# Optimization experiments

Measured on AMD Instinct MI355X. Metric: run time of the kernel, lower is better.

## Reference

```python
import jax, jax.numpy as jnp
import numpy as np

TOP_K = 2
EPS = 1e-06


def setup_inputs() -> dict:
    key = jax.random.key(0)
    k1, k2 = jax.random.split(key)
    x = jax.random.normal(k1, (4, 8192, 1024), dtype=jnp.float32)
    # nn.Linear weight: [num_experts, d_model]
    W = jax.random.normal(k2, (64, 1024), dtype=jnp.float32) * (1.0 / np.sqrt(1024))
    return {"x": x, "W": W}


def reference(x, W):
    # router logits: (b, s, e)
    logits = jnp.einsum('bsd,ed->bse', x, W)
    # top-k selection (values sorted descending, like torch.topk)
    top_vals, top_idx = jax.lax.top_k(logits, TOP_K)
    top_gates = jax.nn.softmax(top_vals, axis=-1)
    # load-balance loss over full softmax probs
    probs = jax.nn.softmax(logits, axis=-1)
    avg_probs = probs.mean(axis=(0, 1))  # (e,)
    # torch.std defaults to unbiased (ddof=1)
    loss = (jnp.std(avg_probs, ddof=1) / (avg_probs.mean() + EPS)) ** 2
    return (top_idx, top_gates, loss)
```

## Files before the change

### kernel.cpp

```cpp
#include <hip/hip_runtime.h>
#include <math.h>
#include <stdint.h>


constexpr int DMODEL = 1024;
constexpr int NEXP   = 64;
constexpr int BM     = 64;
constexpr int BK     = 64;
constexpr int NTOK   = 32768;
constexpr int NTILE  = DMODEL / BK;

constexpr int XS   = 0;
constexpr int XSB  = 64 * 64 * 4;
constexpr int WS   = 32768;
constexpr int WSB  = 3 * 64 * 64 * 2;
constexpr int WCMP = 64 * 64 * 2;
constexpr int LSTR = 68 * 4;

typedef __attribute__((ext_vector_type(8))) short short8;
typedef __attribute__((ext_vector_type(4))) float f32x4;

__device__ __forceinline__ void gload16(const float* g, char* l) {
    __builtin_amdgcn_global_load_lds(
        (const __attribute__((address_space(1))) unsigned int*)g,
        (__attribute__((address_space(3))) unsigned int*)l,
        16, 0, 0);
}

__device__ __forceinline__ void split3(float x, short& h, short& m, short& l) {
    uint32_t u  = __float_as_uint(x);
    uint32_t uh = u & 0xffff0000u;
    float    r  = x - __uint_as_float(uh);
    uint32_t ur = __float_as_uint(r);
    uint32_t um = ur & 0xffff0000u;
    float    r2 = r - __uint_as_float(um);
    h = (short)(uh >> 16);
    m = (short)(um >> 16);
    l = (short)(__float_as_uint(r2) >> 16);
}

__global__ __launch_bounds__(512, 2) void router_kernel(
    const float* __restrict__ x, const float* __restrict__ W,
    float* __restrict__ out, float* __restrict__ expert_sums)
{
    __shared__ __align__(16) char smem[81920];

    const int tid  = threadIdx.x;
    const int lane = tid & 63;
    const int w    = tid >> 6;
    const int mt   = w & 3;
    const int kh   = w >> 2;
    const int tok0 = blockIdx.x * BM;

    f32x4 acc[4];
#pragma unroll
    for (int nt = 0; nt < 4; ++nt) acc[nt] = (f32x4){0.f, 0.f, 0.f, 0.f};

    auto stageX = [&](int buf, int tile) {
#pragma unroll
        for (int i = 0; i < 2; ++i) {
            const int r0 = w * 8 + i * 4;
            const int r  = r0 + (lane >> 4);
            const int c  = lane & 15;
            const float* src = x + (size_t)(tok0 + r) * DMODEL + tile * BK
                                 + ((c ^ (r & 15)) << 2);
            gload16(src, smem + XS + buf * XSB + r0 * 256 + (lane << 4));
        }
    };

    const int we  = tid >> 3;
    const int wc  = tid & 7;
    const int wph = wc ^ (we & 7);
    const float* wgp = W + (size_t)we * DMODEL + wc * 8;

    auto convW = [&](int buf, float4 a, float4 b) {
        short8 sH, sM, sL;
        float v[8] = {a.x, a.y, a.z, a.w, b.x, b.y, b.z, b.w};
#pragma unroll
        for (int j = 0; j < 8; ++j) {
            short h, m, l; split3(v[j], h, m, l);
            sH[j] = h; sM[j] = m; sL[j] = l;
        }
        char* d = smem + WS + buf * WSB + we * 128 + wph * 16;
        *reinterpret_cast<short8*>(d)             = sH;
        *reinterpret_cast<short8*>(d + WCMP)      = sM;
        *reinterpret_cast<short8*>(d + 2 * WCMP)  = sL;
    };

    stageX(0, 0);
    {
        float4 a = *reinterpret_cast<const float4*>(wgp);
        float4 b = *reinterpret_cast<const float4*>(wgp + 4);
        convW(0, a, b);
    }
    __syncthreads();

    int buf = 0;
    for (int tile = 0; tile < NTILE; ++tile) {
        float4 wa, wb;
        if (tile + 1 < NTILE) {
            stageX(buf ^ 1, tile + 1);
            wa = *reinterpret_cast<const float4*>(wgp + (tile + 1) * BK);
            wb = *reinterpret_cast<const float4*>(wgp + (tile + 1) * BK + 4);
        }

        {
            const int ks = kh;
            const int rl = mt * 16 + (lane & 15);
            const int c0 = ks * 8 + (lane >> 4) * 2;
            const char* xrow = smem + XS + buf * XSB + rl * 256;
            const float4 xa = *reinterpret_cast<const float4*>(
                xrow + ((c0 ^ (lane & 15)) << 4));
            const float4 xb = *reinterpret_cast<const float4*>(
                xrow + (((c0 + 1) ^ (lane & 15)) << 4));
            short8 aH, aM, aL;
            {
                float v[8] = {xa.x, xa.y, xa.z, xa.w, xb.x, xb.y, xb.z, xb.w};
#pragma unroll
                for (int j = 0; j < 8; ++j) {
                    short h, m, l; split3(v[j], h, m, l);
                    aH[j] = h; aM[j] = m; aL[j] = l;
                }
            }
#pragma unroll
            for (int nt = 0; nt < 4; ++nt) {
                const int ef = nt * 16 + (lane & 15);
                const int q  = ks * 4 + (lane >> 4);
                const char* wrow = smem + WS + buf * WSB + ef * 128
                                 + ((q ^ (ef & 7)) << 4);
                const short8 bH = *reinterpret_cast<const short8*>(wrow);
                const short8 bM = *reinterpret_cast<const short8*>(wrow + WCMP);
                const short8 bL = *reinterpret_cast<const short8*>(wrow + 2 * WCMP);
                acc[nt] = __builtin_amdgcn_mfma_f32_16x16x32_bf16(aH, bH, acc[nt], 0, 0, 0);
                acc[nt] = __builtin_amdgcn_mfma_f32_16x16x32_bf16(aH, bM, acc[nt], 0, 0, 0);
                acc[nt] = __builtin_amdgcn_mfma_f32_16x16x32_bf16(aM, bH, acc[nt], 0, 0, 0);
                acc[nt] = __builtin_amdgcn_mfma_f32_16x16x32_bf16(aH, bL, acc[nt], 0, 0, 0);
                acc[nt] = __builtin_amdgcn_mfma_f32_16x16x32_bf16(aM, bM, acc[nt], 0, 0, 0);
                acc[nt] = __builtin_amdgcn_mfma_f32_16x16x32_bf16(aL, bH, acc[nt], 0, 0, 0);
            }
        }

        if (tile + 1 < NTILE) convW(buf ^ 1, wa, wb);
        __syncthreads();
        buf ^= 1;
    }

    if (kh == 0) {
#pragma unroll
        for (int nt = 0; nt < 4; ++nt)
#pragma unroll
            for (int r = 0; r < 4; ++r) {
                const int t = mt * 16 + (lane >> 4) * 4 + r;
                const int e = nt * 16 + (lane & 15);
                *reinterpret_cast<float*>(smem + t * LSTR + e * 4) = acc[nt][r];
            }
    }
    __syncthreads();
    if (kh == 1) {
#pragma unroll
        for (int nt = 0; nt < 4; ++nt)
#pragma unroll
            for (int r = 0; r < 4; ++r) {
                const int t = mt * 16 + (lane >> 4) * 4 + r;
                const int e = nt * 16 + (lane & 15);
                float* p = reinterpret_cast<float*>(smem + t * LSTR + e * 4);
                *p += acc[nt][r];
            }
    }
    __syncthreads();

    float* maxArr = reinterpret_cast<float*>(smem + 18432);
    float* invArr = reinterpret_cast<float*>(smem + 18688);
    float* psum   = reinterpret_cast<float*>(smem + 18944);

    if (tid < BM) {
        const char* lrow = smem + tid * LSTR;
        float4 L[16];
#pragma unroll
        for (int i = 0; i < 16; ++i)
            L[i] = *reinterpret_cast<const float4*>(lrow + i * 16);

        float mx = -INFINITY;
#pragma unroll
        for (int i = 0; i < 16; ++i)
            mx = fmaxf(mx, fmaxf(fmaxf(L[i].x, L[i].y), fmaxf(L[i].z, L[i].w)));

        float v0 = -INFINITY, v1 = -INFINITY;
        int   i0 = NEXP, i1 = NEXP;
        float s = 0.f;
#pragma unroll
        for (int i = 0; i < 16; ++i) {
            const float vv[4] = {L[i].x, L[i].y, L[i].z, L[i].w};
#pragma unroll
            for (int c = 0; c < 4; ++c) {
                const float v = vv[c];
                const int  gi = i * 4 + c;
                s += __expf(v - mx);
                if (v > v0) { v1 = v0; i1 = i0; v0 = v; i0 = gi; }
                else if (v > v1) { v1 = v; i1 = gi; }
            }
        }
        maxArr[tid] = mx;
        invArr[tid] = 1.0f / s;

        const float q = __expf(v1 - v0);
        const float d = 1.0f + q;
        const size_t tok = (size_t)tok0 + tid;
        reinterpret_cast<float2*>(out)[tok]            = make_float2((float)i0, (float)i1);
        reinterpret_cast<float2*>(out + 2 * NTOK)[tok] = make_float2(1.0f / d, q / d);
    }
    __syncthreads();

    {
        const int e = tid & 63, grp = tid >> 6;
        float s = 0.f;
#pragma unroll
        for (int i = 0; i < 8; ++i) {
            const int t = grp * 8 + i;
            const float lg = *reinterpret_cast<const float*>(smem + t * LSTR + e * 4);
            s += __expf(lg - maxArr[t]) * invArr[t];
        }
        psum[grp * 64 + e] = s;
    }
    __syncthreads();
    if (tid < 64) {
        float s = 0.f;
#pragma unroll
        for (int g = 0; g < 8; ++g) s += psum[g * 64 + tid];
        atomicAdd(&expert_sums[tid], s);
    }
}

__global__ void loss_kernel(const float* __restrict__ sums, float* __restrict__ out)
{
    const int lane = threadIdx.x;
    float pv = sums[lane] * (1.0f / (float)NTOK);
    float m = pv;
#pragma unroll
    for (int off = 32; off; off >>= 1) m += __shfl_xor(m, off, 64);
    m *= (1.0f / (float)NEXP);
    float d = pv - m;
    float v = d * d;
#pragma unroll
    for (int off = 32; off; off >>= 1) v += __shfl_xor(v, off, 64);
    v *= (1.0f / (float)(NEXP - 1));
    if (lane == 0) {
        float stdv = sqrtf(v);
        float r = stdv / (m + 1e-6f);
        out[4 * NTOK] = r * r;
    }
}

extern "C" void kernel_launch(void* const* d_in, const int* in_sizes, int n_in,
                              void* d_out, int out_size, void* d_ws, size_t ws_size,
                              hipStream_t stream)
{
    const float* x = (const float*)d_in[0];
    const float* W = (const float*)d_in[1];
    float* out  = (float*)d_out;
    float* sums = (float*)d_ws;

    hipMemsetAsync(d_ws, 0, NEXP * sizeof(float), stream);

    hipLaunchKernelGGL(router_kernel, dim3(NTOK / BM), dim3(512), 0, stream,
                       x, W, out, sums);
    hipLaunchKernelGGL(loss_kernel, dim3(1), dim3(64), 0, stream, sums, out);
}
```

Measured before the change: 53.02 us.

## Pre-split W into bf16 triples once and stream tiles via direct-to-LDS loads

Adds a small pre-pass kernel that splits W into hi/mid/lo bf16 components, writes them to workspace in the swizzled LDS tile layout, and has the router kernel load W tiles with global_load_lds instead of converting W per block. This removes the redundant per-block W conversion and its register round-trip. The loop sync changes to explicit vmcnt waits plus raw s_barrier, so the next tile's loads stay in flight during the MFMA work. The cost is an extra kernel launch and workspace traffic. A fallback keeps the old path when the workspace is too small.

```diff
diff --git a/kernel.cpp b/kernel.cpp
--- a/kernel.cpp
+++ b/kernel.cpp
@@ -17,10 +17,13 @@
 constexpr int WCMP = 64 * 64 * 2;
 constexpr int LSTR = 68 * 4;
 
+constexpr size_t WSPLIT_OFF   = 256;
+constexpr size_t WSPLIT_BYTES = (size_t)NTILE * WSB;
+
 typedef __attribute__((ext_vector_type(8))) short short8;
 typedef __attribute__((ext_vector_type(4))) float f32x4;
 
-__device__ __forceinline__ void gload16(const float* g, char* l) {
+__device__ __forceinline__ void gload16(const void* g, void* l) {
     __builtin_amdgcn_global_load_lds(
         (const __attribute__((address_space(1))) unsigned int*)g,
         (__attribute__((address_space(3))) unsigned int*)l,
@@ -39,8 +42,31 @@
     l = (short)(__float_as_uint(r2) >> 16);
 }
 
+__global__ void wsplit_kernel(const float* __restrict__ W, char* __restrict__ dst)
+{
+    const int g = blockIdx.x * 256 + threadIdx.x;
+    const int e = g >> 7;
+    const int c = g & 127;
+    const int tile = c >> 3;
+    const int q    = c & 7;
+    const float* src = W + (size_t)e * DMODEL + c * 8;
+    const float4 a = *reinterpret_cast<const float4*>(src);
+    const float4 b = *reinterpret_cast<const float4*>(src + 4);
+    short8 sH, sM, sL;
+    const float v[8] = {a.x, a.y, a.z, a.w, b.x, b.y, b.z, b.w};
+#pragma unroll
+    for (int j = 0; j < 8; ++j) {
+        short h, m, l; split3(v[j], h, m, l);
+        sH[j] = h; sM[j] = m; sL[j] = l;
+    }
+    char* base = dst + (size_t)tile * WSB + e * 128 + ((q ^ (e & 7)) << 4);
+    *reinterpret_cast<short8*>(base)            = sH;
+    *reinterpret_cast<short8*>(base + WCMP)     = sM;
+    *reinterpret_cast<short8*>(base + 2 * WCMP) = sL;
+}
+
 __global__ __launch_bounds__(512, 2) void router_kernel(
-    const float* __restrict__ x, const float* __restrict__ W,
+    const float* __restrict__ x, const char* __restrict__ wsAll,
     float* __restrict__ out, float* __restrict__ expert_sums)
 {
     __shared__ __align__(16) char smem[81920];
@@ -67,42 +93,28 @@
             gload16(src, smem + XS + buf * XSB + r0 * 256 + (lane << 4));
         }
     };
-
-    const int we  = tid >> 3;
-    const int wc  = tid & 7;
-    const int wph = wc ^ (we & 7);
-    const float* wgp = W + (size_t)we * DMODEL + wc * 8;
-
-    auto convW = [&](int buf, float4 a, float4 b) {
-        short8 sH, sM, sL;
-        float v[8] = {a.x, a.y, a.z, a.w, b.x, b.y, b.z, b.w};
-#pragma unroll
-        for (int j = 0; j < 8; ++j) {
-            short h, m, l; split3(v[j], h, m, l);
-            sH[j] = h; sM[j] = m; sL[j] = l;
-        }
-        char* d = smem + WS + buf * WSB + we * 128 + wph * 16;
-        *reinterpret_cast<short8*>(d)             = sH;
-        *reinterpret_cast<short8*>(d + WCMP)      = sM;
-        *reinterpret_cast<short8*>(d + 2 * WCMP)  = sL;
+    auto stageW = [&](int buf, int tile) {
+        const char* src = wsAll + (size_t)tile * WSB + w * 1024 + (lane << 4);
+        char* dst = smem + WS + buf * WSB + w * 1024 + (lane << 4);
+#pragma unroll
+        for (int j = 0; j < 3; ++j)
+            gload16(src + j * WCMP, dst + j * WCMP);
     };
 
     stageX(0, 0);
-    {
-        float4 a = *reinterpret_cast<const float4*>(wgp);
-        float4 b = *reinterpret_cast<const float4*>(wgp + 4);
-        convW(0, a, b);
-    }
-    __syncthreads();
+    stageW(0, 0);
 
     int buf = 0;
     for (int tile = 0; tile < NTILE; ++tile) {
-        float4 wa, wb;
         if (tile + 1 < NTILE) {
             stageX(buf ^ 1, tile + 1);
-            wa = *reinterpret_cast<const float4*>(wgp + (tile + 1) * BK);
-            wb = *reinterpret_cast<const float4*>(wgp + (tile + 1) * BK + 4);
-        }
+            stageW(buf ^ 1, tile + 1);
+            asm volatile("s_waitcnt vmcnt(5)" ::: "memory");
+        } else {
+            asm volatile("s_waitcnt vmcnt(0)" ::: "memory");
+        }
+        __builtin_amdgcn_sched_barrier(0);
+        __builtin_amdgcn_s_barrier();
 
         {
             const int ks = kh;
@@ -139,9 +151,7 @@
                 acc[nt] = __builtin_amdgcn_mfma_f32_16x16x32_bf16(aL, bH, acc[nt], 0, 0, 0);
             }
         }
-
-        if (tile + 1 < NTILE) convW(buf ^ 1, wa, wb);
-        __syncthreads();
+        __builtin_amdgcn_s_barrier();
         buf ^= 1;
     }
 
@@ -211,6 +221,192 @@
     }
     __syncthreads();
 
+    {
+        const int e = tid & 63, grp = tid >> 6;
+        float s = 0.f;
+#pragma unroll
+        for (int i = 0; i < 8; ++i) {
+            const int t = grp * 8 + i;
+            const float lg = *reinterpret_cast<const float*>(smem + t * LSTR + e * 4);
+            s += __expf(lg - maxArr[t]) * invArr[t];
+        }
+        psum[grp * 64 + e] = s;
+    }
+    __syncthreads();
+    if (tid < 64) {
+        float s = 0.f;
+#pragma unroll
+        for (int g = 0; g < 8; ++g) s += psum[g * 64 + tid];
+        atomicAdd(&expert_sums[tid], s);
+    }
+}
+
+__global__ __launch_bounds__(512, 2) void router_fallback(
+    const float* __restrict__ x, const float* __restrict__ W,
+    float* __restrict__ out, float* __restrict__ expert_sums)
+{
+    __shared__ __align__(16) char smem[81920];
+
+    const int tid  = threadIdx.x;
+    const int lane = tid & 63;
+    const int w    = tid >> 6;
+    const int mt   = w & 3;
+    const int kh   = w >> 2;
+    const int tok0 = blockIdx.x * BM;
+
+    f32x4 acc[4];
+#pragma unroll
+    for (int nt = 0; nt < 4; ++nt) acc[nt] = (f32x4){0.f, 0.f, 0.f, 0.f};
+
+    auto stageX = [&](int buf, int tile) {
+#pragma unroll
+        for (int i = 0; i < 2; ++i) {
+            const int r0 = w * 8 + i * 4;
+            const int r  = r0 + (lane >> 4);
+            const int c  = lane & 15;
+            const float* src = x + (size_t)(tok0 + r) * DMODEL + tile * BK
+                                 + ((c ^ (r & 15)) << 2);
+            gload16(src, smem + XS + buf * XSB + r0 * 256 + (lane << 4));
+        }
+    };
+
+    const int we  = tid >> 3;
+    const int wc  = tid & 7;
+    const int wph = wc ^ (we & 7);
+    const float* wgp = W + (size_t)we * DMODEL + wc * 8;
+
+    auto convW = [&](int buf, float4 a, float4 b) {
+        short8 sH, sM, sL;
+        float v[8] = {a.x, a.y, a.z, a.w, b.x, b.y, b.z, b.w};
+#pragma unroll
+        for (int j = 0; j < 8; ++j) {
+            short h, m, l; split3(v[j], h, m, l);
+            sH[j] = h; sM[j] = m; sL[j] = l;
+        }
+        char* d = smem + WS + buf * WSB + we * 128 + wph * 16;
+        *reinterpret_cast<short8*>(d)             = sH;
+        *reinterpret_cast<short8*>(d + WCMP)      = sM;
+        *reinterpret_cast<short8*>(d + 2 * WCMP)  = sL;
+    };
+
+    stageX(0, 0);
+    {
+        float4 a = *reinterpret_cast<const float4*>(wgp);
+        float4 b = *reinterpret_cast<const float4*>(wgp + 4);
+        convW(0, a, b);
+    }
+    __syncthreads();
+
+    int buf = 0;
+    for (int tile = 0; tile < NTILE; ++tile) {
+        float4 wa, wb;
+        if (tile + 1 < NTILE) {
+            stageX(buf ^ 1, tile + 1);
+            wa = *reinterpret_cast<const float4*>(wgp + (tile + 1) * BK);
+            wb = *reinterpret_cast<const float4*>(wgp + (tile + 1) * BK + 4);
+        }
+        {
+            const int ks = kh;
+            const int rl = mt * 16 + (lane & 15);
+            const int c0 = ks * 8 + (lane >> 4) * 2;
+            const char* xrow = smem + XS + buf * XSB + rl * 256;
+            const float4 xa = *reinterpret_cast<const float4*>(
+                xrow + ((c0 ^ (lane & 15)) << 4));
+            const float4 xb = *reinterpret_cast<const float4*>(
+                xrow + (((c0 + 1) ^ (lane & 15)) << 4));
+            short8 aH, aM, aL;
+            {
+                float v[8] = {xa.x, xa.y, xa.z, xa.w, xb.x, xb.y, xb.z, xb.w};
+#pragma unroll
+                for (int j = 0; j < 8; ++j) {
+                    short h, m, l; split3(v[j], h, m, l);
+                    aH[j] = h; aM[j] = m; aL[j] = l;
+                }
+            }
+#pragma unroll
+            for (int nt = 0; nt < 4; ++nt) {
+                const int ef = nt * 16 + (lane & 15);
+                const int q  = ks * 4 + (lane >> 4);
+                const char* wrow = smem + WS + buf * WSB + ef * 128
+                                 + ((q ^ (ef & 7)) << 4);
+                const short8 bH = *reinterpret_cast<const short8*>(wrow);
+                const short8 bM = *reinterpret_cast<const short8*>(wrow + WCMP);
+                const short8 bL = *reinterpret_cast<const short8*>(wrow + 2 * WCMP);
+                acc[nt] = __builtin_amdgcn_mfma_f32_16x16x32_bf16(aH, bH, acc[nt], 0, 0, 0);
+                acc[nt] = __builtin_amdgcn_mfma_f32_16x16x32_bf16(aH, bM, acc[nt], 0, 0, 0);
+                acc[nt] = __builtin_amdgcn_mfma_f32_16x16x32_bf16(aM, bH, acc[nt], 0, 0, 0);
+                acc[nt] = __builtin_amdgcn_mfma_f32_16x16x32_bf16(aH, bL, acc[nt], 0, 0, 0);
+                acc[nt] = __builtin_amdgcn_mfma_f32_16x16x32_bf16(aM, bM, acc[nt], 0, 0, 0);
+                acc[nt] = __builtin_amdgcn_mfma_f32_16x16x32_bf16(aL, bH, acc[nt], 0, 0, 0);
+            }
+        }
+        if (tile + 1 < NTILE) convW(buf ^ 1, wa, wb);
+        __syncthreads();
+        buf ^= 1;
+    }
+
+    if (kh == 0) {
+#pragma unroll
+        for (int nt = 0; nt < 4; ++nt)
+#pragma unroll
+            for (int r = 0; r < 4; ++r) {
+                const int t = mt * 16 + (lane >> 4) * 4 + r;
+                const int e = nt * 16 + (lane & 15);
+                *reinterpret_cast<float*>(smem + t * LSTR + e * 4) = acc[nt][r];
+            }
+    }
+    __syncthreads();
+    if (kh == 1) {
+#pragma unroll
+        for (int nt = 0; nt < 4; ++nt)
+#pragma unroll
+            for (int r = 0; r < 4; ++r) {
+                const int t = mt * 16 + (lane >> 4) * 4 + r;
+                const int e = nt * 16 + (lane & 15);
+                float* p = reinterpret_cast<float*>(smem + t * LSTR + e * 4);
+                *p += acc[nt][r];
+            }
+    }
+    __syncthreads();
+
+    float* maxArr = reinterpret_cast<float*>(smem + 18432);
+    float* invArr = reinterpret_cast<float*>(smem + 18688);
+    float* psum   = reinterpret_cast<float*>(smem + 18944);
+
+    if (tid < BM) {
+        const char* lrow = smem + tid * LSTR;
+        float4 L[16];
+#pragma unroll
+        for (int i = 0; i < 16; ++i)
+            L[i] = *reinterpret_cast<const float4*>(lrow + i * 16);
+        float mx = -INFINITY;
+#pragma unroll
+        for (int i = 0; i < 16; ++i)
+            mx = fmaxf(mx, fmaxf(fmaxf(L[i].x, L[i].y), fmaxf(L[i].z, L[i].w)));
+        float v0 = -INFINITY, v1 = -INFINITY;
+        int   i0 = NEXP, i1 = NEXP;
+        float s = 0.f;
+#pragma unroll
+        for (int i = 0; i < 16; ++i) {
+            const float vv[4] = {L[i].x, L[i].y, L[i].z, L[i].w};
+#pragma unroll
+            for (int c = 0; c < 4; ++c) {
+                const float v = vv[c];
+                const int  gi = i * 4 + c;
+                s += __expf(v - mx);
+                if (v > v0) { v1 = v0; i1 = i0; v0 = v; i0 = gi; }
+                else if (v > v1) { v1 = v; i1 = gi; }
+            }
+        }
+        maxArr[tid] = mx;
+        invArr[tid] = 1.0f / s;
+        const float q = __expf(v1 - v0);
+        const float d = 1.0f + q;
+        const size_t tok = (size_t)tok0 + tid;
+        reinterpret_cast<float2*>(out)[tok]            = make_float2((float)i0, (float)i1);
+        reinterpret_cast<float2*>(out + 2 * NTOK)[tok] = make_float2(1.0f / d, q / d);
+    }
+    __syncthreads();
     {
         const int e = tid & 63, grp = tid >> 6;
         float s = 0.f;
@@ -260,9 +456,16 @@
     float* out  = (float*)d_out;
     float* sums = (float*)d_ws;
 
-    hipMemsetAsync(d_ws, 0, NEXP * sizeof(float), stream);
-
-    hipLaunchKernelGGL(router_kernel, dim3(NTOK / BM), dim3(512), 0, stream,
-                       x, W, out, sums);
+    hipMemsetAsync(d_ws, 0, 256, stream);
+
+    if (ws_size >= WSPLIT_OFF + WSPLIT_BYTES) {
+        char* wsAll = (char*)d_ws + WSPLIT_OFF;
+        hipLaunchKernelGGL(wsplit_kernel, dim3(32), dim3(256), 0, stream, W, wsAll);
+        hipLaunchKernelGGL(router_kernel, dim3(NTOK / BM), dim3(512), 0, stream,
+                           x, wsAll, out, sums);
+    } else {
+        hipLaunchKernelGGL(router_fallback, dim3(NTOK / BM), dim3(512), 0, stream,
+                           x, W, out, sums);
+    }
     hipLaunchKernelGGL(loss_kernel, dim3(1), dim3(64), 0, stream, sums, out);
 }
```

Result: faster. 51.57 us (-2.7%).
